# Kernel optimization log

Measured on AMD Instinct MI355X. Metric: run time of the kernel, lower is better.

## Reference

```python
import jax, jax.numpy as jnp
import numpy as np

EPS = 1e-5

def _act_quant(x):
    # per-token int8 absmax quantization with straight-through estimator
    scale = 127.0 / jnp.clip(jnp.max(jnp.abs(x), axis=-1, keepdims=True), EPS, None)
    q = jnp.clip(jnp.round(x * scale), -128.0, 127.0) / scale
    return x + jax.lax.stop_gradient(q - x)

def _weight_quant(w):
    # per-tensor ternary (1.58-bit) quantization with STE
    scale = 1.0 / jnp.clip(jnp.mean(jnp.abs(w)), EPS, None)
    q = jnp.clip(jnp.round(w * scale), -1.0, 1.0) / scale
    return w + jax.lax.stop_gradient(q - w)

def _bitlinear(x, w, b):
    y = jnp.einsum('bsd,od->bso', _act_quant(x), _weight_quant(w))
    return y + b

def setup_inputs() -> dict:
    key = jax.random.key(0)
    k1, k2, k3, k4, k5 = jax.random.split(key, 5)
    B, S, D, F = 8, 4096, 1024, 3072
    return {
        'x': jax.random.normal(k1, (B, S, D), dtype=jnp.float32),
        'up_w': jax.random.normal(k2, (F, D), dtype=jnp.float32) * 0.125,
        'up_b': jax.random.normal(k3, (F,), dtype=jnp.float32) * 0.01,
        'down_w': jax.random.normal(k4, (D, F), dtype=jnp.float32) * 0.125,
        'down_b': jax.random.normal(k5, (D,), dtype=jnp.float32) * 0.01,
    }

def reference(x, up_w, up_b, down_w, down_b):
    hidden = _bitlinear(x, up_w, up_b)          # [B,S,3072]
    hidden = jnp.square(jax.nn.relu(hidden))    # relu(h)^2
    return _bitlinear(hidden, down_w, down_b)   # [B,S,1024]
```

## Files before the change

### kernel.cpp

```cpp
#include <hip/hip_runtime.h>
#include <hip/hip_bf16.h>
#include <stdint.h>

#define EPS 1e-5f

typedef int v4i __attribute__((ext_vector_type(4)));
typedef int v16i __attribute__((ext_vector_type(16)));
typedef const __attribute__((address_space(1))) void g_void;
typedef __attribute__((address_space(3))) void l_void;

__device__ inline float block_sum64x4(float v) {
    __shared__ float s[4];
#pragma unroll
    for (int o = 32; o; o >>= 1) v += __shfl_xor(v, o, 64);
    if ((threadIdx.x & 63) == 0) s[threadIdx.x >> 6] = v;
    __syncthreads();
    return s[0] + s[1] + s[2] + s[3];
}

__global__ __launch_bounds__(256) void abs_sum_part_k(const float4* __restrict__ w,
                                                      int n4, float* __restrict__ part) {
    float s = 0.0f;
    for (int i = blockIdx.x * 256 + threadIdx.x; i < n4; i += 1024 * 256) {
        float4 v = w[i];
        s += fabsf(v.x) + fabsf(v.y) + fabsf(v.z) + fabsf(v.w);
    }
    s = block_sum64x4(s);
    if (threadIdx.x == 0) part[blockIdx.x] = s;
}

__global__ __launch_bounds__(256) void abs_sum_final_k(const float* __restrict__ parts,
                                                       float* __restrict__ sums) {
    const float* p = parts + blockIdx.x * 1024;
    const int t = threadIdx.x;
    float s = p[t] + p[t + 256] + p[t + 512] + p[t + 768];
    s = block_sum64x4(s);
    if (t == 0) sums[blockIdx.x] = s;
}

__global__ __launch_bounds__(256) void wquant_k(const float4* __restrict__ w,
                                                char4* __restrict__ q,
                                                const float* __restrict__ sum) {
    const float mean = fmaxf(sum[0] * (1.0f / 3145728.0f), EPS);
    const float scale = 1.0f / mean;
    const int i = blockIdx.x * 256 + threadIdx.x;
    float4 v = w[i];
    char4 c;
    c.x = (signed char)(int)fmaxf(fminf(rintf(v.x * scale), 1.0f), -1.0f);
    c.y = (signed char)(int)fmaxf(fminf(rintf(v.y * scale), 1.0f), -1.0f);
    c.z = (signed char)(int)fmaxf(fminf(rintf(v.z * scale), 1.0f), -1.0f);
    c.w = (signed char)(int)fmaxf(fminf(rintf(v.w * scale), 1.0f), -1.0f);
    q[i] = c;
}

__global__ __launch_bounds__(256) void aquant_k(const float4* __restrict__ x,
                                                char4* __restrict__ q,
                                                float* __restrict__ deq) {
    const int wv = threadIdx.x >> 6, lane = threadIdx.x & 63;
    const size_t row = (size_t)blockIdx.x * 4 + wv;
    const float4* xr = x + row * 256;
    float4 v[4];
    float m = 0.0f;
#pragma unroll
    for (int j = 0; j < 4; ++j) {
        v[j] = xr[j * 64 + lane];
        m = fmaxf(m, fmaxf(fmaxf(fabsf(v[j].x), fabsf(v[j].y)),
                           fmaxf(fabsf(v[j].z), fabsf(v[j].w))));
    }
#pragma unroll
    for (int o = 32; o; o >>= 1) m = fmaxf(m, __shfl_xor(m, o, 64));
    const float mc = fmaxf(m, EPS);
    const float sc = 127.0f / mc;
    char4* qr = q + row * 256;
#pragma unroll
    for (int j = 0; j < 4; ++j) {
        char4 c;
        c.x = (signed char)(int)fmaxf(fminf(rintf(v[j].x * sc), 127.0f), -128.0f);
        c.y = (signed char)(int)fmaxf(fminf(rintf(v[j].y * sc), 127.0f), -128.0f);
        c.z = (signed char)(int)fmaxf(fminf(rintf(v[j].z * sc), 127.0f), -128.0f);
        c.w = (signed char)(int)fmaxf(fminf(rintf(v[j].w * sc), 127.0f), -128.0f);
        qr[j * 64 + lane] = c;
    }
    if (lane == 0) deq[row] = mc / 127.0f;
}

__global__ __launch_bounds__(256) void hquant_k(unsigned short* __restrict__ hid,
                                                float* __restrict__ deq) {
    const int wv = threadIdx.x >> 6, lane = threadIdx.x & 63;
    const size_t row = (size_t)blockIdx.x * 4 + wv;
    unsigned short* rp = hid + row * 3072;
    float vals[48];
    float m = 0.0f;
#pragma unroll
    for (int j = 0; j < 6; ++j) {
        const uint4 u = ((const uint4*)rp)[j * 64 + lane];
        uint32_t uu[4] = {u.x, u.y, u.z, u.w};
#pragma unroll
        for (int i = 0; i < 4; ++i) {
            vals[j * 8 + 2 * i]     = __uint_as_float(uu[i] << 16);
            vals[j * 8 + 2 * i + 1] = __uint_as_float(uu[i] & 0xFFFF0000u);
        }
#pragma unroll
        for (int i = 0; i < 8; ++i) m = fmaxf(m, vals[j * 8 + i]);
    }
#pragma unroll
    for (int o = 32; o; o >>= 1) m = fmaxf(m, __shfl_xor(m, o, 64));
    const float mc = fmaxf(m, EPS);
    const float sc = 127.0f / mc;
#pragma unroll
    for (int j = 0; j < 6; ++j) {
        uint32_t p0 = 0, p1 = 0;
#pragma unroll
        for (int i = 0; i < 4; ++i) {
            int c = (int)fminf(rintf(vals[j * 8 + i] * sc), 127.0f);
            p0 |= (uint32_t)(c & 255) << (8 * i);
        }
#pragma unroll
        for (int i = 0; i < 4; ++i) {
            int c = (int)fminf(rintf(vals[j * 8 + 4 + i] * sc), 127.0f);
            p1 |= (uint32_t)(c & 255) << (8 * i);
        }
        uint2 pk; pk.x = p0; pk.y = p1;
        ((uint2*)rp)[j * 64 + lane] = pk;
    }
    if (lane == 0) deq[row] = mc / 127.0f;
}

template <int K, int NTILES, bool RELU2, typename OutT>
__global__ __launch_bounds__(256, 2) void gemm_i8(
    const int8_t* __restrict__ A, int lda,
    const int8_t* __restrict__ B, int ldb,
    OutT* __restrict__ O, int ldo,
    const float* __restrict__ rowDeq,
    const float* __restrict__ sumPtr,
    const float* __restrict__ bias) {
    constexpr int NT = K >> 6;
    __shared__ __align__(16) char lds[3][24576];
    const int t = threadIdx.x;
    const int lane = t & 63;
    const int w = t >> 6;
    const int xcd = blockIdx.x & 7;
    const int sb = blockIdx.x >> 3;
    const int bm = xcd + 8 * (sb / NTILES);
    const int bn = sb % NTILES;
    const long m0 = (long)bm * 128;
    const long n0 = (long)bn * 256;

    v16i acc[2][4];
#pragma unroll
    for (int i = 0; i < 2; ++i)
#pragma unroll
        for (int j = 0; j < 4; ++j) acc[i][j] = (v16i)(0);

    const int mloc = (w >> 1) * 64;
    const int nloc = (w & 1) * 128;
    const int r32 = lane & 31;
    const int h = lane >> 5;

    const int srow = lane >> 2;
    const int scS = ((lane & 3) ^ ((lane >> 3) & 3)) * 16;
    const int8_t* paS0 = A + (m0 + w * 32 + srow) * (long)lda + scS;
    const int8_t* paS1 = paS0 + 16 * (long)lda;
    const int8_t* pbS0 = B + (n0 + w * 64 + srow) * (long)ldb + scS;
    const int8_t* pbS1 = pbS0 + 16 * (long)ldb;
    const int8_t* pbS2 = pbS0 + 32 * (long)ldb;
    const int8_t* pbS3 = pbS0 + 48 * (long)ldb;

    const int swz = (r32 >> 1) & 3;
    const char* rdA0 = &lds[0][0] + (mloc + r32) * 64 + ((h ^ swz) * 16);
    const char* rdA1 = &lds[0][0] + (mloc + r32) * 64 + (((2 + h) ^ swz) * 16);
    const char* rdB0 = &lds[0][0] + 8192 + (nloc + r32) * 64 + ((h ^ swz) * 16);
    const char* rdB1 = &lds[0][0] + 8192 + (nloc + r32) * 64 + (((2 + h) ^ swz) * 16);

    auto STAGE = [&](int tt) {
        char* buf = &lds[0][0] + (tt % 3) * 24576;
        const long ko = (long)tt << 6;
        __builtin_amdgcn_global_load_lds((g_void*)(paS0 + ko),
                                         (l_void*)(buf + w * 2048), 16, 0, 0);
        __builtin_amdgcn_global_load_lds((g_void*)(paS1 + ko),
                                         (l_void*)(buf + w * 2048 + 1024), 16, 0, 0);
        __builtin_amdgcn_global_load_lds((g_void*)(pbS0 + ko),
                                         (l_void*)(buf + 8192 + w * 4096), 16, 0, 0);
        __builtin_amdgcn_global_load_lds((g_void*)(pbS1 + ko),
                                         (l_void*)(buf + 8192 + w * 4096 + 1024), 16, 0, 0);
        __builtin_amdgcn_global_load_lds((g_void*)(pbS2 + ko),
                                         (l_void*)(buf + 8192 + w * 4096 + 2048), 16, 0, 0);
        __builtin_amdgcn_global_load_lds((g_void*)(pbS3 + ko),
                                         (l_void*)(buf + 8192 + w * 4096 + 3072), 16, 0, 0);
    };

    STAGE(0);
    STAGE(1);
    asm volatile("s_waitcnt vmcnt(6)" ::: "memory");
    __builtin_amdgcn_s_barrier();
    __builtin_amdgcn_sched_barrier(0);

#pragma unroll
    for (int tt = 0; tt < NT; ++tt) {
        const int bo = (tt % 3) * 24576;
        if (tt + 2 < NT) STAGE(tt + 2);
        v4i af[2][2], bf[2][4];
#pragma unroll
        for (int ks = 0; ks < 2; ++ks) {
            const char* rA = ks ? rdA1 : rdA0;
            const char* rB = ks ? rdB1 : rdB0;
#pragma unroll
            for (int mt = 0; mt < 2; ++mt)
                af[ks][mt] = *(const v4i*)(rA + bo + mt * 2048);
#pragma unroll
            for (int nt = 0; nt < 4; ++nt)
                bf[ks][nt] = *(const v4i*)(rB + bo + nt * 2048);
        }
#pragma unroll
        for (int ks = 0; ks < 2; ++ks)
#pragma unroll
            for (int mt = 0; mt < 2; ++mt)
#pragma unroll
                for (int nt = 0; nt < 4; ++nt)
                    acc[mt][nt] = __builtin_amdgcn_mfma_i32_32x32x32_i8(
                        af[ks][mt], bf[ks][nt], acc[mt][nt], 0, 0, 0);
        if (tt + 1 < NT) {
            if (tt + 2 < NT) asm volatile("s_waitcnt vmcnt(6) lgkmcnt(0)" ::: "memory");
            else             asm volatile("s_waitcnt vmcnt(0) lgkmcnt(0)" ::: "memory");
            __builtin_amdgcn_s_barrier();
            __builtin_amdgcn_sched_barrier(0);
        }
    }

    const float wdeq = fmaxf(sumPtr[0] * (1.0f / 3145728.0f), EPS);
#pragma unroll
    for (int mt = 0; mt < 2; ++mt) {
#pragma unroll
        for (int g = 0; g < 4; ++g) {
#pragma unroll
            for (int rr = 0; rr < 4; ++rr) {
                const long row = m0 + mloc + mt * 32 + g * 8 + h * 4 + rr;
                const float rs = rowDeq[row] * wdeq;
#pragma unroll
                for (int nt = 0; nt < 4; ++nt) {
                    const long col = n0 + nloc + nt * 32 + r32;
                    float val = (float)acc[mt][nt][g * 4 + rr] * rs + bias[col];
                    if (RELU2) {
                        val = fmaxf(val, 0.0f);
                        val = val * val;
                    }
                    O[row * (long)ldo + col] = (OutT)val;
                }
            }
        }
    }
}

extern "C" void kernel_launch(void* const* d_in, const int* in_sizes, int n_in,
                              void* d_out, int out_size, void* d_ws, size_t ws_size,
                              hipStream_t stream) {
    const float* x      = (const float*)d_in[0];
    const float* up_w   = (const float*)d_in[1];
    const float* up_b   = (const float*)d_in[2];
    const float* down_w = (const float*)d_in[3];
    const float* down_b = (const float*)d_in[4];

    char* ws = (char*)d_ws;
    float*  sums   = (float*)ws;
    float*  parts  = (float*)(ws + 256);
    int8_t* qw_dn  = (int8_t*)(ws + 256 + 8192);
    float*  deqh   = (float*)(ws + 256 + 8192 + 3145728);
    __hip_bfloat16* hidden = (__hip_bfloat16*)(ws + 256 + 8192 + 3145728 + 131072);

    int8_t* qx    = (int8_t*)d_out;
    int8_t* qw_up = qx + 33554432;
    float*  deqx  = (float*)(qx + 33554432 + 3145728);

    abs_sum_part_k<<<1024, 256, 0, stream>>>((const float4*)up_w, 786432, parts);
    abs_sum_part_k<<<1024, 256, 0, stream>>>((const float4*)down_w, 786432, parts + 1024);
    abs_sum_final_k<<<2, 256, 0, stream>>>(parts, sums);

    wquant_k<<<3072, 256, 0, stream>>>((const float4*)up_w, (char4*)qw_up, &sums[0]);
    wquant_k<<<3072, 256, 0, stream>>>((const float4*)down_w, (char4*)qw_dn, &sums[1]);
    aquant_k<<<8192, 256, 0, stream>>>((const float4*)x, (char4*)qx, deqx);

    gemm_i8<1024, 12, true, __hip_bfloat16><<<3072, 256, 0, stream>>>(
        qx, 1024, qw_up, 1024, hidden, 3072, deqx, &sums[0], up_b);
    hquant_k<<<8192, 256, 0, stream>>>((unsigned short*)hidden, deqh);
    gemm_i8<3072, 4, false, float><<<1024, 256, 0, stream>>>(
        (const int8_t*)hidden, 6144, qw_dn, 3072, (float*)d_out, 1024,
        deqh, &sums[1], down_b);
}
```

Before: 523.7 us.

## Switch GEMM to double-buffered LDS for 3 blocks/CU and merge weight kernels

The int8 GEMM drops from a triple-buffered to a double-buffered LDS pipeline (72KB to 48KB shared memory) and raises launch bounds to 3 blocks per CU. It prefetches only one stage ahead and waits on all outstanding loads each iteration. The point is to raise occupancy so other resident blocks hide latency, at the cost of less prefetch depth within each block. The two abs-sum launches and the two weight-quant launches are also each merged into one launch to cut launch overhead.

```diff
diff --git a/kernel.cpp b/kernel.cpp
--- a/kernel.cpp
+++ b/kernel.cpp
@@ -18,10 +18,13 @@
     return s[0] + s[1] + s[2] + s[3];
 }
 
-__global__ __launch_bounds__(256) void abs_sum_part_k(const float4* __restrict__ w,
-                                                      int n4, float* __restrict__ part) {
+__global__ __launch_bounds__(256) void abs_sum_part_k(const float4* __restrict__ w0,
+                                                      const float4* __restrict__ w1,
+                                                      float* __restrict__ part) {
+    const int half = blockIdx.x >> 10;
+    const float4* w = half ? w1 : w0;
     float s = 0.0f;
-    for (int i = blockIdx.x * 256 + threadIdx.x; i < n4; i += 1024 * 256) {
+    for (int i = (blockIdx.x & 1023) * 256 + threadIdx.x; i < 786432; i += 1024 * 256) {
         float4 v = w[i];
         s += fabsf(v.x) + fabsf(v.y) + fabsf(v.z) + fabsf(v.w);
     }
@@ -38,12 +41,17 @@
     if (t == 0) sums[blockIdx.x] = s;
 }
 
-__global__ __launch_bounds__(256) void wquant_k(const float4* __restrict__ w,
-                                                char4* __restrict__ q,
-                                                const float* __restrict__ sum) {
-    const float mean = fmaxf(sum[0] * (1.0f / 3145728.0f), EPS);
+__global__ __launch_bounds__(256) void wquant_k(const float4* __restrict__ w0,
+                                                const float4* __restrict__ w1,
+                                                char4* __restrict__ q0,
+                                                char4* __restrict__ q1,
+                                                const float* __restrict__ sums) {
+    const int half = (blockIdx.x >= 3072) ? 1 : 0;
+    const float4* w = half ? w1 : w0;
+    char4* q = half ? q1 : q0;
+    const float mean = fmaxf(sums[half] * (1.0f / 3145728.0f), EPS);
     const float scale = 1.0f / mean;
-    const int i = blockIdx.x * 256 + threadIdx.x;
+    const int i = (blockIdx.x - half * 3072) * 256 + threadIdx.x;
     float4 v = w[i];
     char4 c;
     c.x = (signed char)(int)fmaxf(fminf(rintf(v.x * scale), 1.0f), -1.0f);
@@ -127,7 +135,7 @@
 }
 
 template <int K, int NTILES, bool RELU2, typename OutT>
-__global__ __launch_bounds__(256, 2) void gemm_i8(
+__global__ __launch_bounds__(256, 3) void gemm_i8(
     const int8_t* __restrict__ A, int lda,
     const int8_t* __restrict__ B, int ldb,
     OutT* __restrict__ O, int ldo,
@@ -135,7 +143,7 @@
     const float* __restrict__ sumPtr,
     const float* __restrict__ bias) {
     constexpr int NT = K >> 6;
-    __shared__ __align__(16) char lds[3][24576];
+    __shared__ __align__(16) char lds[2][24576];
     const int t = threadIdx.x;
     const int lane = t & 63;
     const int w = t >> 6;
@@ -173,7 +181,7 @@
     const char* rdB1 = &lds[0][0] + 8192 + (nloc + r32) * 64 + (((2 + h) ^ swz) * 16);
 
     auto STAGE = [&](int tt) {
-        char* buf = &lds[0][0] + (tt % 3) * 24576;
+        char* buf = &lds[0][0] + (tt & 1) * 24576;
         const long ko = (long)tt << 6;
         __builtin_amdgcn_global_load_lds((g_void*)(paS0 + ko),
                                          (l_void*)(buf + w * 2048), 16, 0, 0);
@@ -190,15 +198,15 @@
     };
 
     STAGE(0);
-    STAGE(1);
-    asm volatile("s_waitcnt vmcnt(6)" ::: "memory");
+    asm volatile("s_waitcnt vmcnt(0)" ::: "memory");
     __builtin_amdgcn_s_barrier();
     __builtin_amdgcn_sched_barrier(0);
 
 #pragma unroll
     for (int tt = 0; tt < NT; ++tt) {
-        const int bo = (tt % 3) * 24576;
-        if (tt + 2 < NT) STAGE(tt + 2);
+        const int bo = (tt & 1) * 24576;
+        if (tt + 1 < NT) STAGE(tt + 1);
+        __builtin_amdgcn_sched_barrier(0);
         v4i af[2][2], bf[2][4];
 #pragma unroll
         for (int ks = 0; ks < 2; ++ks) {
@@ -220,8 +228,7 @@
                     acc[mt][nt] = __builtin_amdgcn_mfma_i32_32x32x32_i8(
                         af[ks][mt], bf[ks][nt], acc[mt][nt], 0, 0, 0);
         if (tt + 1 < NT) {
-            if (tt + 2 < NT) asm volatile("s_waitcnt vmcnt(6) lgkmcnt(0)" ::: "memory");
-            else             asm volatile("s_waitcnt vmcnt(0) lgkmcnt(0)" ::: "memory");
+            asm volatile("s_waitcnt vmcnt(0) lgkmcnt(0)" ::: "memory");
             __builtin_amdgcn_s_barrier();
             __builtin_amdgcn_sched_barrier(0);
         }
@@ -271,12 +278,12 @@
     int8_t* qw_up = qx + 33554432;
     float*  deqx  = (float*)(qx + 33554432 + 3145728);
 
-    abs_sum_part_k<<<1024, 256, 0, stream>>>((const float4*)up_w, 786432, parts);
-    abs_sum_part_k<<<1024, 256, 0, stream>>>((const float4*)down_w, 786432, parts + 1024);
+    abs_sum_part_k<<<2048, 256, 0, stream>>>((const float4*)up_w,
+                                             (const float4*)down_w, parts);
     abs_sum_final_k<<<2, 256, 0, stream>>>(parts, sums);
 
-    wquant_k<<<3072, 256, 0, stream>>>((const float4*)up_w, (char4*)qw_up, &sums[0]);
-    wquant_k<<<3072, 256, 0, stream>>>((const float4*)down_w, (char4*)qw_dn, &sums[1]);
+    wquant_k<<<6144, 256, 0, stream>>>((const float4*)up_w, (const float4*)down_w,
+                                       (char4*)qw_up, (char4*)qw_dn, sums);
     aquant_k<<<8192, 256, 0, stream>>>((const float4*)x, (char4*)qx, deqx);
 
     gemm_i8<1024, 12, true, __hip_bfloat16><<<3072, 256, 0, stream>>>(
```

Measured after the change: 518.2 us. Within noise of the previous version (-1.0%).
